# Kernel optimization log

Measured on AMD Instinct MI355X. Metric: run time of the kernel, lower is better.

The kernel has to match this reference:

```python
import jax, jax.numpy as jnp
import numpy as np

DK = 64

def setup_inputs() -> dict:
    key = jax.random.key(0)
    kx, kq, kk, kv = jax.random.split(key, 4)
    B, T, DM, DV = 256, 256, 384, 64
    x = jax.random.normal(kx, (B, T, DM), dtype=jnp.float32)
    s = 1.0 / np.sqrt(DM)
    W_q = jax.random.normal(kq, (DM, DK), dtype=jnp.float32) * s
    W_k = jax.random.normal(kk, (DM, DK), dtype=jnp.float32) * s
    W_v = jax.random.normal(kv, (DM, DV), dtype=jnp.float32) * s
    return {"x": x, "W_q": W_q, "W_k": W_k, "W_v": W_v}

def reference(x, W_q, W_k, W_v):
    # x: [B, T, dm]; projections to [B, T, dk]/[B, T, dv]
    q = jnp.einsum('btc,ck->btk', x, W_q)
    k = jnp.einsum('btc,ck->btk', x, W_k)
    v = jnp.einsum('btc,cv->btv', x, W_v)
    scale = k.shape[-1] ** (-0.5)
    wei = jnp.einsum('btk,bsk->bts', q, k) * scale  # [B, T, T]
    T = x.shape[1]
    causal = jnp.tril(jnp.ones((T, T), dtype=bool))
    wei = jnp.where(causal, wei, -jnp.inf)
    wei = jax.nn.softmax(wei, axis=-1)
    # dropout omitted (eval mode / deterministic reference)
    out = jnp.einsum('bts,bsv->btv', wei, v)
    return out
```

## Files before the change

### kernel.cpp

```cpp
#include <hip/hip_runtime.h>


typedef __attribute__((ext_vector_type(8))) short short8;
typedef __attribute__((ext_vector_type(4))) float floatx4;

__device__ inline unsigned short f2bf(float f) {
  union { float f; unsigned u; } v; v.f = f;
  unsigned r = v.u + 0x7FFFu + ((v.u >> 16) & 1u);
  return (unsigned short)(r >> 16);
}

__device__ inline void glds16(const void* g, void* l) {
  __builtin_amdgcn_global_load_lds(
      (const __attribute__((address_space(1))) void*)g,
      (__attribute__((address_space(3))) void*)l, 16, 0, 0);
}

__global__ void wt_kernel(const float* __restrict__ wq, const float* __restrict__ wk,
                          const float* __restrict__ wv, unsigned short* __restrict__ wt) {
  int idx = blockIdx.x * 256 + threadIdx.x;
  if (idx >= 3 * 64 * 384) return;
  int mat = idx / (64 * 384);
  int rem = idx % (64 * 384);
  int n = rem / 384, k = rem % 384;
  const float* w = (mat == 0) ? wq : ((mat == 1) ? wk : wv);
  wt[idx] = f2bf(w[k * 64 + n]);
}

__global__ __launch_bounds__(1024) void fused_kernel(
    const float* __restrict__ x, const unsigned short* __restrict__ wt,
    float* __restrict__ out) {
  __shared__ __align__(16) unsigned short wb[2][3 * 192 * 32];
  __shared__ __align__(16) unsigned short sK[256 * 72];
  __shared__ __align__(16) unsigned short sVT[64 * 264];

  int tid = threadIdx.x, lane = tid & 63, w = tid >> 6;
  int m = lane & 15, q = lane >> 4;
  int b = blockIdx.x;
  const float* xb = x + (size_t)b * 256 * 384;

  auto stage = [&](int mega, int buf) {
#pragma unroll
    for (int t = 0; t < 3; ++t) {
      int i = w + 16 * t;
      if (i < 36) {
        int kc = i / 12, sub = i % 12;
        int c = sub * 16 + (lane >> 2), g = lane & 3;
        glds16(wt + (size_t)c * 384 + (mega * 3 + kc) * 32 + g * 8,
               (void*)&wb[buf][kc * 6144 + sub * 512]);
      }
    }
  };

  floatx4 z = {0.f, 0.f, 0.f, 0.f};
  floatx4 acc[12];
#pragma unroll
  for (int nt = 0; nt < 12; ++nt) acc[nt] = z;

  stage(0, 0);
#pragma unroll
  for (int mega = 0; mega < 4; ++mega) {
    int buf = mega & 1;
    __syncthreads();
    if (mega < 3) stage(mega + 1, buf ^ 1);

#pragma unroll
    for (int kc = 0; kc < 3; ++kc) {
      int ks = mega * 3 + kc;
      const float* ap = xb + (size_t)(w * 16 + m) * 384 + ks * 32 + q * 8;
      float4 f0 = *(const float4*)ap;
      float4 f1 = *(const float4*)(ap + 4);
      short8 af;
      af[0] = (short)f2bf(f0.x); af[1] = (short)f2bf(f0.y);
      af[2] = (short)f2bf(f0.z); af[3] = (short)f2bf(f0.w);
      af[4] = (short)f2bf(f1.x); af[5] = (short)f2bf(f1.y);
      af[6] = (short)f2bf(f1.z); af[7] = (short)f2bf(f1.w);

      const unsigned short* wbk = &wb[buf][kc * 6144];
#pragma unroll
      for (int nt = 0; nt < 12; ++nt) {
        short8 bf = *(const short8*)&wbk[(nt * 16 + m) * 32 + q * 8];
        acc[nt] = __builtin_amdgcn_mfma_f32_16x16x32_bf16(af, bf, acc[nt], 0, 0, 0);
      }
    }
  }

  unsigned short* scr = &wb[0][0] + w * 1152;
#pragma unroll
  for (int nt = 0; nt < 8; ++nt) {
#pragma unroll
    for (int j = 0; j < 4; ++j) {
      unsigned short val = f2bf(acc[nt][j]);
      int lrow = q * 4 + j;
      if (nt < 4) scr[lrow * 72 + nt * 16 + m] = val;
      else        sK[(w * 16 + lrow) * 72 + (nt - 4) * 16 + m] = val;
    }
  }
#pragma unroll
  for (int nt = 8; nt < 12; ++nt) {
    ushort4 pv;
    pv.x = f2bf(acc[nt][0]); pv.y = f2bf(acc[nt][1]);
    pv.z = f2bf(acc[nt][2]); pv.w = f2bf(acc[nt][3]);
    *(ushort4*)&sVT[((nt - 8) * 16 + m) * 264 + w * 16 + q * 4] = pv;
  }

  short8 qf0 = *(const short8*)(scr + m * 72 + q * 8);
  short8 qf1 = *(const short8*)(scr + m * 72 + 32 + q * 8);

  __syncthreads();

  floatx4 sacc[16];
#pragma unroll
  for (int nt = 0; nt < 16; ++nt) {
    if (nt > w) continue;
    short8 kb0 = *(const short8*)(sK + (nt * 16 + m) * 72 + q * 8);
    short8 kb1 = *(const short8*)(sK + (nt * 16 + m) * 72 + 32 + q * 8);
    floatx4 t = __builtin_amdgcn_mfma_f32_16x16x32_bf16(qf0, kb0, z, 0, 0, 0);
    sacc[nt] = __builtin_amdgcn_mfma_f32_16x16x32_bf16(qf1, kb1, t, 0, 0, 0);
  }

  const float CSC = 0.18033688011112042f;
  float inv_[4];
  int rbase = w * 16 + q * 4;
#pragma unroll
  for (int j = 0; j < 4; ++j) {
    int rg = rbase + j;
    float sum = 0.f;
#pragma unroll
    for (int nt = 0; nt < 16; ++nt) {
      if (nt > w) continue;
      int col = nt * 16 + m;
      float p = (col <= rg) ? exp2f(sacc[nt][j] * CSC) : 0.f;
      sacc[nt][j] = p;
      sum += p;
    }
    sum += __shfl_xor(sum, 1);
    sum += __shfl_xor(sum, 2);
    sum += __shfl_xor(sum, 4);
    sum += __shfl_xor(sum, 8);
    inv_[j] = 1.f / sum;
  }

  floatx4 o[4];
#pragma unroll
  for (int vt = 0; vt < 4; ++vt) o[vt] = z;
#pragma unroll
  for (int c = 0; c < 4; ++c) {
    if (4 * c > w) continue;
#pragma unroll
    for (int t = 0; t < 4; ++t) {
      int nt = 4 * c + t;
#pragma unroll
      for (int j = 0; j < 4; ++j) {
        unsigned short pv = (nt <= w) ? f2bf(sacc[nt][j] * inv_[j]) : (unsigned short)0;
        scr[(q * 4 + j) * 72 + t * 16 + m] = pv;
      }
    }
    short8 pf0 = *(const short8*)(scr + m * 72 + q * 8);
    short8 pf1 = *(const short8*)(scr + m * 72 + 32 + q * 8);
#pragma unroll
    for (int vt = 0; vt < 4; ++vt) {
      short8 vb0 = *(const short8*)(sVT + (vt * 16 + m) * 264 + c * 64 + q * 8);
      short8 vb1 = *(const short8*)(sVT + (vt * 16 + m) * 264 + c * 64 + 32 + q * 8);
      o[vt] = __builtin_amdgcn_mfma_f32_16x16x32_bf16(pf0, vb0, o[vt], 0, 0, 0);
      o[vt] = __builtin_amdgcn_mfma_f32_16x16x32_bf16(pf1, vb1, o[vt], 0, 0, 0);
    }
  }

  float* op = out + ((size_t)b * 256 + w * 16) * 64;
#pragma unroll
  for (int vt = 0; vt < 4; ++vt)
#pragma unroll
    for (int j = 0; j < 4; ++j)
      op[(q * 4 + j) * 64 + vt * 16 + m] = o[vt][j];
}

extern "C" void kernel_launch(void* const* d_in, const int* in_sizes, int n_in,
                              void* d_out, int out_size, void* d_ws, size_t ws_size,
                              hipStream_t stream) {
  const float* x  = (const float*)d_in[0];
  const float* wq = (const float*)d_in[1];
  const float* wk = (const float*)d_in[2];
  const float* wv = (const float*)d_in[3];
  float* out = (float*)d_out;

  unsigned short* wt = (unsigned short*)d_ws;

  wt_kernel<<<288, 256, 0, stream>>>(wq, wk, wv, wt);
  fused_kernel<<<256, 1024, 0, stream>>>(x, wt, out);
}
```

Measured before the change: 171.4 us.

## Split fused attention into QKV projection and load-balanced attention kernels

```diff
diff --git a/kernel.cpp b/kernel.cpp
--- a/kernel.cpp
+++ b/kernel.cpp
@@ -27,28 +27,24 @@
   wt[idx] = f2bf(w[k * 64 + n]);
 }
 
-__global__ __launch_bounds__(1024) void fused_kernel(
+__global__ __launch_bounds__(256, 4) void qkv_kernel(
     const float* __restrict__ x, const unsigned short* __restrict__ wt,
-    float* __restrict__ out) {
-  __shared__ __align__(16) unsigned short wb[2][3 * 192 * 32];
-  __shared__ __align__(16) unsigned short sK[256 * 72];
-  __shared__ __align__(16) unsigned short sVT[64 * 264];
+    unsigned short* __restrict__ Qg, unsigned short* __restrict__ Kg,
+    unsigned short* __restrict__ VTg) {
+  __shared__ __align__(16) unsigned short wb[2][6144];
 
   int tid = threadIdx.x, lane = tid & 63, w = tid >> 6;
   int m = lane & 15, q = lane >> 4;
-  int b = blockIdx.x;
-  const float* xb = x + (size_t)b * 256 * 384;
-
-  auto stage = [&](int mega, int buf) {
+  size_t R0 = (size_t)blockIdx.x * 64;
+  const float* ap0 = x + (R0 + (size_t)(w * 16 + m)) * 384 + q * 8;
+
+  auto stage = [&](int ks, int buf) {
 #pragma unroll
     for (int t = 0; t < 3; ++t) {
-      int i = w + 16 * t;
-      if (i < 36) {
-        int kc = i / 12, sub = i % 12;
-        int c = sub * 16 + (lane >> 2), g = lane & 3;
-        glds16(wt + (size_t)c * 384 + (mega * 3 + kc) * 32 + g * 8,
-               (void*)&wb[buf][kc * 6144 + sub * 512]);
-      }
+      int sub = w * 3 + t;
+      int c = sub * 16 + (lane >> 2), g = lane & 3;
+      glds16(wt + (size_t)c * 384 + ks * 32 + g * 8,
+             (void*)&wb[buf][sub * 512]);
     }
   };
 
@@ -59,120 +55,130 @@
 
   stage(0, 0);
 #pragma unroll
-  for (int mega = 0; mega < 4; ++mega) {
-    int buf = mega & 1;
+  for (int ks = 0; ks < 12; ++ks) {
+    int buf = ks & 1;
     __syncthreads();
-    if (mega < 3) stage(mega + 1, buf ^ 1);
-
-#pragma unroll
-    for (int kc = 0; kc < 3; ++kc) {
-      int ks = mega * 3 + kc;
-      const float* ap = xb + (size_t)(w * 16 + m) * 384 + ks * 32 + q * 8;
-      float4 f0 = *(const float4*)ap;
-      float4 f1 = *(const float4*)(ap + 4);
-      short8 af;
-      af[0] = (short)f2bf(f0.x); af[1] = (short)f2bf(f0.y);
-      af[2] = (short)f2bf(f0.z); af[3] = (short)f2bf(f0.w);
-      af[4] = (short)f2bf(f1.x); af[5] = (short)f2bf(f1.y);
-      af[6] = (short)f2bf(f1.z); af[7] = (short)f2bf(f1.w);
-
-      const unsigned short* wbk = &wb[buf][kc * 6144];
-#pragma unroll
-      for (int nt = 0; nt < 12; ++nt) {
-        short8 bf = *(const short8*)&wbk[(nt * 16 + m) * 32 + q * 8];
-        acc[nt] = __builtin_amdgcn_mfma_f32_16x16x32_bf16(af, bf, acc[nt], 0, 0, 0);
-      }
-    }
-  }
+    if (ks < 11) stage(ks + 1, buf ^ 1);
+
+    float4 f0 = *(const float4*)(ap0 + ks * 32);
+    float4 f1 = *(const float4*)(ap0 + ks * 32 + 4);
+    short8 af;
+    af[0] = (short)f2bf(f0.x); af[1] = (short)f2bf(f0.y);
+    af[2] = (short)f2bf(f0.z); af[3] = (short)f2bf(f0.w);
+    af[4] = (short)f2bf(f1.x); af[5] = (short)f2bf(f1.y);
+    af[6] = (short)f2bf(f1.z); af[7] = (short)f2bf(f1.w);
+
+#pragma unroll
+    for (int nt = 0; nt < 12; ++nt) {
+      short8 bf = *(const short8*)&wb[buf][(nt * 16 + m) * 32 + q * 8];
+      acc[nt] = __builtin_amdgcn_mfma_f32_16x16x32_bf16(af, bf, acc[nt], 0, 0, 0);
+    }
+  }
+  __syncthreads();
 
   unsigned short* scr = &wb[0][0] + w * 1152;
 #pragma unroll
-  for (int nt = 0; nt < 8; ++nt) {
-#pragma unroll
-    for (int j = 0; j < 4; ++j) {
-      unsigned short val = f2bf(acc[nt][j]);
-      int lrow = q * 4 + j;
-      if (nt < 4) scr[lrow * 72 + nt * 16 + m] = val;
-      else        sK[(w * 16 + lrow) * 72 + (nt - 4) * 16 + m] = val;
-    }
-  }
+  for (int pass = 0; pass < 2; ++pass) {
+#pragma unroll
+    for (int nt = 0; nt < 4; ++nt) {
+#pragma unroll
+      for (int j = 0; j < 4; ++j)
+        scr[(q * 4 + j) * 72 + nt * 16 + m] = f2bf(acc[pass * 4 + nt][j]);
+    }
+    unsigned short* dst = (pass == 0 ? Qg : Kg) + (R0 + (size_t)(w * 16)) * 64;
+#pragma unroll
+    for (int pr = 0; pr < 2; ++pr) {
+      int sr = pr * 8 + (lane >> 3);
+      short8 row = *(const short8*)(scr + sr * 72 + (lane & 7) * 8);
+      *(short8*)(dst + sr * 64 + (lane & 7) * 8) = row;
+    }
+  }
+
+  int bb = (int)(R0 >> 8);
+  int tok0 = (int)(R0 & 255) + w * 16 + q * 4;
 #pragma unroll
   for (int nt = 8; nt < 12; ++nt) {
     ushort4 pv;
     pv.x = f2bf(acc[nt][0]); pv.y = f2bf(acc[nt][1]);
     pv.z = f2bf(acc[nt][2]); pv.w = f2bf(acc[nt][3]);
-    *(ushort4*)&sVT[((nt - 8) * 16 + m) * 264 + w * 16 + q * 4] = pv;
-  }
-
-  short8 qf0 = *(const short8*)(scr + m * 72 + q * 8);
-  short8 qf1 = *(const short8*)(scr + m * 72 + 32 + q * 8);
-
-  __syncthreads();
-
-  floatx4 sacc[16];
-#pragma unroll
-  for (int nt = 0; nt < 16; ++nt) {
-    if (nt > w) continue;
-    short8 kb0 = *(const short8*)(sK + (nt * 16 + m) * 72 + q * 8);
-    short8 kb1 = *(const short8*)(sK + (nt * 16 + m) * 72 + 32 + q * 8);
-    floatx4 t = __builtin_amdgcn_mfma_f32_16x16x32_bf16(qf0, kb0, z, 0, 0, 0);
-    sacc[nt] = __builtin_amdgcn_mfma_f32_16x16x32_bf16(qf1, kb1, t, 0, 0, 0);
-  }
+    *(ushort4*)(VTg + ((size_t)bb * 64 + (nt - 8) * 16 + m) * 256 + tok0) = pv;
+  }
+}
+
+__global__ __launch_bounds__(256, 4) void attn_kernel(
+    const unsigned short* __restrict__ Qg, const unsigned short* __restrict__ Kg,
+    const unsigned short* __restrict__ VTg, float* __restrict__ out) {
+  __shared__ __align__(16) unsigned short ps[4][640];
+
+  int tid = threadIdx.x, lane = tid & 63, w = tid >> 6;
+  int m = lane & 15, q = lane >> 4;
+  int b = blockIdx.x >> 2, qd = blockIdx.x & 3;
+  int r = (w >> 1) * 8 + ((w & 1) ? 7 - qd : qd);
+
+  const unsigned short* Qb = Qg + ((size_t)b * 256 + r * 16) * 64;
+  const unsigned short* Kb = Kg + (size_t)b * 256 * 64;
+  const unsigned short* Vb = VTg + (size_t)b * 64 * 256;
+  unsigned short* scr = ps[w];
+
+  short8 qf0 = *(const short8*)(Qb + m * 64 + q * 8);
+  short8 qf1 = *(const short8*)(Qb + m * 64 + 32 + q * 8);
+
+  floatx4 z = {0.f, 0.f, 0.f, 0.f};
+  floatx4 o[4];
+#pragma unroll
+  for (int vt = 0; vt < 4; ++vt) o[vt] = z;
+  float sum[4] = {0.f, 0.f, 0.f, 0.f};
 
   const float CSC = 0.18033688011112042f;
+  int rg = r * 16 + q * 4;
+  int np = (r >> 1) + 1;
+
+  for (int p = 0; p < np; ++p) {
+    const unsigned short* k0 = Kb + (size_t)(2 * p) * 16 * 64;
+    short8 ka0 = *(const short8*)(k0 + m * 64 + q * 8);
+    short8 ka1 = *(const short8*)(k0 + m * 64 + 32 + q * 8);
+    short8 kb0 = *(const short8*)(k0 + (16 + m) * 64 + q * 8);
+    short8 kb1 = *(const short8*)(k0 + (16 + m) * 64 + 32 + q * 8);
+    floatx4 s0 = __builtin_amdgcn_mfma_f32_16x16x32_bf16(qf0, ka0, z, 0, 0, 0);
+    s0 = __builtin_amdgcn_mfma_f32_16x16x32_bf16(qf1, ka1, s0, 0, 0, 0);
+    floatx4 s1 = __builtin_amdgcn_mfma_f32_16x16x32_bf16(qf0, kb0, z, 0, 0, 0);
+    s1 = __builtin_amdgcn_mfma_f32_16x16x32_bf16(qf1, kb1, s1, 0, 0, 0);
+
+    int c0 = 2 * p * 16 + m;
+#pragma unroll
+    for (int j = 0; j < 4; ++j) {
+      float p0 = (c0 <= rg + j) ? exp2f(s0[j] * CSC) : 0.f;
+      float p1 = (c0 + 16 <= rg + j) ? exp2f(s1[j] * CSC) : 0.f;
+      sum[j] += p0 + p1;
+      scr[(q * 4 + j) * 40 + m] = f2bf(p0);
+      scr[(q * 4 + j) * 40 + 16 + m] = f2bf(p1);
+    }
+    short8 pf = *(const short8*)(scr + m * 40 + q * 8);
+    const unsigned short* vp = Vb + p * 32 + q * 8;
+#pragma unroll
+    for (int vt = 0; vt < 4; ++vt) {
+      short8 vb = *(const short8*)(vp + (size_t)(vt * 16 + m) * 256);
+      o[vt] = __builtin_amdgcn_mfma_f32_16x16x32_bf16(pf, vb, o[vt], 0, 0, 0);
+    }
+  }
+
   float inv_[4];
-  int rbase = w * 16 + q * 4;
 #pragma unroll
   for (int j = 0; j < 4; ++j) {
-    int rg = rbase + j;
-    float sum = 0.f;
-#pragma unroll
-    for (int nt = 0; nt < 16; ++nt) {
-      if (nt > w) continue;
-      int col = nt * 16 + m;
-      float p = (col <= rg) ? exp2f(sacc[nt][j] * CSC) : 0.f;
-      sacc[nt][j] = p;
-      sum += p;
-    }
-    sum += __shfl_xor(sum, 1);
-    sum += __shfl_xor(sum, 2);
-    sum += __shfl_xor(sum, 4);
-    sum += __shfl_xor(sum, 8);
-    inv_[j] = 1.f / sum;
-  }
-
-  floatx4 o[4];
-#pragma unroll
-  for (int vt = 0; vt < 4; ++vt) o[vt] = z;
-#pragma unroll
-  for (int c = 0; c < 4; ++c) {
-    if (4 * c > w) continue;
-#pragma unroll
-    for (int t = 0; t < 4; ++t) {
-      int nt = 4 * c + t;
-#pragma unroll
-      for (int j = 0; j < 4; ++j) {
-        unsigned short pv = (nt <= w) ? f2bf(sacc[nt][j] * inv_[j]) : (unsigned short)0;
-        scr[(q * 4 + j) * 72 + t * 16 + m] = pv;
-      }
-    }
-    short8 pf0 = *(const short8*)(scr + m * 72 + q * 8);
-    short8 pf1 = *(const short8*)(scr + m * 72 + 32 + q * 8);
-#pragma unroll
-    for (int vt = 0; vt < 4; ++vt) {
-      short8 vb0 = *(const short8*)(sVT + (vt * 16 + m) * 264 + c * 64 + q * 8);
-      short8 vb1 = *(const short8*)(sVT + (vt * 16 + m) * 264 + c * 64 + 32 + q * 8);
-      o[vt] = __builtin_amdgcn_mfma_f32_16x16x32_bf16(pf0, vb0, o[vt], 0, 0, 0);
-      o[vt] = __builtin_amdgcn_mfma_f32_16x16x32_bf16(pf1, vb1, o[vt], 0, 0, 0);
-    }
-  }
-
-  float* op = out + ((size_t)b * 256 + w * 16) * 64;
+    float s = sum[j];
+    s += __shfl_xor(s, 1);
+    s += __shfl_xor(s, 2);
+    s += __shfl_xor(s, 4);
+    s += __shfl_xor(s, 8);
+    inv_[j] = 1.f / s;
+  }
+
+  float* op = out + ((size_t)b * 256 + r * 16) * 64;
 #pragma unroll
   for (int vt = 0; vt < 4; ++vt)
 #pragma unroll
     for (int j = 0; j < 4; ++j)
-      op[(q * 4 + j) * 64 + vt * 16 + m] = o[vt][j];
+      op[(q * 4 + j) * 64 + vt * 16 + m] = o[vt][j] * inv_[j];
 }
 
 extern "C" void kernel_launch(void* const* d_in, const int* in_sizes, int n_in,
@@ -184,8 +190,13 @@
   const float* wv = (const float*)d_in[3];
   float* out = (float*)d_out;
 
-  unsigned short* wt = (unsigned short*)d_ws;
+  unsigned char* ws = (unsigned char*)d_ws;
+  unsigned short* wt = (unsigned short*)ws;
+  unsigned short* Qg = (unsigned short*)(ws + (1u << 20));
+  unsigned short* Kg = (unsigned short*)(ws + (1u << 20) + (1u << 23));
+  unsigned short* VTg = (unsigned short*)(ws + (1u << 20) + (2u << 23));
 
   wt_kernel<<<288, 256, 0, stream>>>(wq, wk, wv, wt);
-  fused_kernel<<<256, 1024, 0, stream>>>(x, wt, out);
-}
+  qkv_kernel<<<1024, 256, 0, stream>>>(x, wt, Qg, Kg, VTg);
+  attn_kernel<<<1024, 256, 0, stream>>>(Qg, Kg, VTg, out);
+}
```

New measurement: 194.7 us. 1.14x slower.

## Split each batch across two 512-thread blocks with balanced causal row-tile pairing

Applied to the files above, without the earlier changes.

```diff
diff --git a/kernel.cpp b/kernel.cpp
--- a/kernel.cpp
+++ b/kernel.cpp
@@ -27,108 +27,134 @@
   wt[idx] = f2bf(w[k * 64 + n]);
 }
 
-__global__ __launch_bounds__(1024) void fused_kernel(
+__global__ __launch_bounds__(512, 4) void fused_kernel(
     const float* __restrict__ x, const unsigned short* __restrict__ wt,
     float* __restrict__ out) {
-  __shared__ __align__(16) unsigned short wb[2][3 * 192 * 32];
-  __shared__ __align__(16) unsigned short sK[256 * 72];
-  __shared__ __align__(16) unsigned short sVT[64 * 264];
+  __shared__ __align__(16) unsigned short U[37888];
 
   int tid = threadIdx.x, lane = tid & 63, w = tid >> 6;
   int m = lane & 15, q = lane >> 4;
-  int b = blockIdx.x;
+
+  int i = blockIdx.x;
+  int xcd = i & 7, jj = i >> 3;
+  int b = xcd * 32 + (jj >> 1);
+  int h = jj & 1;
   const float* xb = x + (size_t)b * 256 * 384;
 
-  auto stage = [&](int mega, int buf) {
-#pragma unroll
-    for (int t = 0; t < 3; ++t) {
-      int i = w + 16 * t;
-      if (i < 36) {
-        int kc = i / 12, sub = i % 12;
+  int ta = 2 * w + ((w ^ h) & 1);
+  int tb = 4 * w + 1 - ta;
+
+  auto stage = [&](int ks, int buf) {
+#pragma unroll
+    for (int t = 0; t < 2; ++t) {
+      int sub = w + 8 * t;
+      if (sub < 12) {
         int c = sub * 16 + (lane >> 2), g = lane & 3;
-        glds16(wt + (size_t)c * 384 + (mega * 3 + kc) * 32 + g * 8,
-               (void*)&wb[buf][kc * 6144 + sub * 512]);
+        glds16(wt + (size_t)c * 384 + ks * 32 + g * 8,
+               (void*)&U[buf * 6144 + sub * 512]);
       }
     }
   };
 
   floatx4 z = {0.f, 0.f, 0.f, 0.f};
-  floatx4 acc[12];
-#pragma unroll
-  for (int nt = 0; nt < 12; ++nt) acc[nt] = z;
+  floatx4 aA[12], aB[8];
+#pragma unroll
+  for (int nt = 0; nt < 12; ++nt) aA[nt] = z;
+#pragma unroll
+  for (int nt = 0; nt < 8; ++nt) aB[nt] = z;
+
+  const float* rowa = xb + (size_t)(ta * 16 + m) * 384 + q * 8;
+  const float* rowb = xb + (size_t)(tb * 16 + m) * 384 + q * 8;
 
   stage(0, 0);
 #pragma unroll
-  for (int mega = 0; mega < 4; ++mega) {
-    int buf = mega & 1;
+  for (int ks = 0; ks < 12; ++ks) {
+    int buf = ks & 1;
     __syncthreads();
-    if (mega < 3) stage(mega + 1, buf ^ 1);
-
-#pragma unroll
-    for (int kc = 0; kc < 3; ++kc) {
-      int ks = mega * 3 + kc;
-      const float* ap = xb + (size_t)(w * 16 + m) * 384 + ks * 32 + q * 8;
-      float4 f0 = *(const float4*)ap;
-      float4 f1 = *(const float4*)(ap + 4);
-      short8 af;
-      af[0] = (short)f2bf(f0.x); af[1] = (short)f2bf(f0.y);
-      af[2] = (short)f2bf(f0.z); af[3] = (short)f2bf(f0.w);
-      af[4] = (short)f2bf(f1.x); af[5] = (short)f2bf(f1.y);
-      af[6] = (short)f2bf(f1.z); af[7] = (short)f2bf(f1.w);
-
-      const unsigned short* wbk = &wb[buf][kc * 6144];
-#pragma unroll
-      for (int nt = 0; nt < 12; ++nt) {
-        short8 bf = *(const short8*)&wbk[(nt * 16 + m) * 32 + q * 8];
-        acc[nt] = __builtin_amdgcn_mfma_f32_16x16x32_bf16(af, bf, acc[nt], 0, 0, 0);
-      }
-    }
-  }
-
-  unsigned short* scr = &wb[0][0] + w * 1152;
-#pragma unroll
-  for (int nt = 0; nt < 8; ++nt) {
+    if (ks < 11) stage(ks + 1, buf ^ 1);
+
+    float4 a0 = *(const float4*)(rowa + ks * 32);
+    float4 a1 = *(const float4*)(rowa + ks * 32 + 4);
+    float4 b0 = *(const float4*)(rowb + ks * 32);
+    float4 b1 = *(const float4*)(rowb + ks * 32 + 4);
+    short8 afA, afB;
+    afA[0] = (short)f2bf(a0.x); afA[1] = (short)f2bf(a0.y);
+    afA[2] = (short)f2bf(a0.z); afA[3] = (short)f2bf(a0.w);
+    afA[4] = (short)f2bf(a1.x); afA[5] = (short)f2bf(a1.y);
+    afA[6] = (short)f2bf(a1.z); afA[7] = (short)f2bf(a1.w);
+    afB[0] = (short)f2bf(b0.x); afB[1] = (short)f2bf(b0.y);
+    afB[2] = (short)f2bf(b0.z); afB[3] = (short)f2bf(b0.w);
+    afB[4] = (short)f2bf(b1.x); afB[5] = (short)f2bf(b1.y);
+    afB[6] = (short)f2bf(b1.z); afB[7] = (short)f2bf(b1.w);
+
+#pragma unroll
+    for (int nt = 0; nt < 12; ++nt) {
+      short8 bf = *(const short8*)&U[buf * 6144 + (nt * 16 + m) * 32 + q * 8];
+      aA[nt] = __builtin_amdgcn_mfma_f32_16x16x32_bf16(afA, bf, aA[nt], 0, 0, 0);
+      if (nt >= 4)
+        aB[nt - 4] = __builtin_amdgcn_mfma_f32_16x16x32_bf16(afB, bf, aB[nt - 4], 0, 0, 0);
+    }
+  }
+
+  unsigned short* qs = U + 16384 + w * 1152;
+#pragma unroll
+  for (int nt = 0; nt < 4; ++nt)
+#pragma unroll
+    for (int j = 0; j < 4; ++j)
+      qs[(q * 4 + j) * 72 + nt * 16 + m] = f2bf(aA[nt][j]);
+  short8 qf0 = *(const short8*)(qs + m * 72 + q * 8);
+  short8 qf1 = *(const short8*)(qs + m * 72 + 32 + q * 8);
+
+  __syncthreads();
+
+  char* Uc = (char*)U;
+#pragma unroll
+  for (int n4 = 0; n4 < 4; ++n4) {
 #pragma unroll
     for (int j = 0; j < 4; ++j) {
-      unsigned short val = f2bf(acc[nt][j]);
-      int lrow = q * 4 + j;
-      if (nt < 4) scr[lrow * 72 + nt * 16 + m] = val;
-      else        sK[(w * 16 + lrow) * 72 + (nt - 4) * 16 + m] = val;
-    }
-  }
-#pragma unroll
-  for (int nt = 8; nt < 12; ++nt) {
-    ushort4 pv;
-    pv.x = f2bf(acc[nt][0]); pv.y = f2bf(acc[nt][1]);
-    pv.z = f2bf(acc[nt][2]); pv.w = f2bf(acc[nt][3]);
-    *(ushort4*)&sVT[((nt - 8) * 16 + m) * 264 + w * 16 + q * 4] = pv;
-  }
-
-  short8 qf0 = *(const short8*)(scr + m * 72 + q * 8);
-  short8 qf1 = *(const short8*)(scr + m * 72 + 32 + q * 8);
+      int ra = ta * 16 + q * 4 + j, ca = n4 * 16 + m;
+      int bya = (ra * 128 + ca * 2) ^ ((ra & 7) << 4);
+      *(unsigned short*)(Uc + bya) = f2bf(aA[4 + n4][j]);
+      int rb = tb * 16 + q * 4 + j;
+      int byb = (rb * 128 + ca * 2) ^ ((rb & 7) << 4);
+      *(unsigned short*)(Uc + byb) = f2bf(aB[n4][j]);
+    }
+    int vrow = n4 * 16 + m;
+    ushort4 pa, pb;
+    pa.x = f2bf(aA[8 + n4][0]); pa.y = f2bf(aA[8 + n4][1]);
+    pa.z = f2bf(aA[8 + n4][2]); pa.w = f2bf(aA[8 + n4][3]);
+    pb.x = f2bf(aB[4 + n4][0]); pb.y = f2bf(aB[4 + n4][1]);
+    pb.z = f2bf(aB[4 + n4][2]); pb.w = f2bf(aB[4 + n4][3]);
+    int bva = (vrow * 512 + (ta * 16 + q * 4) * 2) ^ ((vrow & 7) << 4);
+    int bvb = (vrow * 512 + (tb * 16 + q * 4) * 2) ^ ((vrow & 7) << 4);
+    *(ushort4*)(Uc + 32768 + bva) = pa;
+    *(ushort4*)(Uc + 32768 + bvb) = pb;
+  }
 
   __syncthreads();
 
+  int r = ta;
   floatx4 sacc[16];
 #pragma unroll
   for (int nt = 0; nt < 16; ++nt) {
-    if (nt > w) continue;
-    short8 kb0 = *(const short8*)(sK + (nt * 16 + m) * 72 + q * 8);
-    short8 kb1 = *(const short8*)(sK + (nt * 16 + m) * 72 + 32 + q * 8);
+    if (nt > r) continue;
+    int by0 = (((nt * 16 + m) * 128) + q * 16) ^ ((m & 7) << 4);
+    short8 kb0 = *(const short8*)(Uc + by0);
+    short8 kb1 = *(const short8*)(Uc + (by0 ^ 64));
     floatx4 t = __builtin_amdgcn_mfma_f32_16x16x32_bf16(qf0, kb0, z, 0, 0, 0);
     sacc[nt] = __builtin_amdgcn_mfma_f32_16x16x32_bf16(qf1, kb1, t, 0, 0, 0);
   }
 
   const float CSC = 0.18033688011112042f;
   float inv_[4];
-  int rbase = w * 16 + q * 4;
+  int rbase = r * 16 + q * 4;
 #pragma unroll
   for (int j = 0; j < 4; ++j) {
     int rg = rbase + j;
     float sum = 0.f;
 #pragma unroll
     for (int nt = 0; nt < 16; ++nt) {
-      if (nt > w) continue;
+      if (nt > r) continue;
       int col = nt * 16 + m;
       float p = (col <= rg) ? exp2f(sacc[nt][j] * CSC) : 0.f;
       sacc[nt][j] = p;
@@ -141,33 +167,32 @@
     inv_[j] = 1.f / sum;
   }
 
+  unsigned short* ps = U + 32768 + w * 640;
   floatx4 o[4];
 #pragma unroll
   for (int vt = 0; vt < 4; ++vt) o[vt] = z;
 #pragma unroll
-  for (int c = 0; c < 4; ++c) {
-    if (4 * c > w) continue;
-#pragma unroll
-    for (int t = 0; t < 4; ++t) {
-      int nt = 4 * c + t;
+  for (int c2 = 0; c2 < 8; ++c2) {
+    if (2 * c2 > r) continue;
+#pragma unroll
+    for (int t = 0; t < 2; ++t) {
+      int nt = 2 * c2 + t;
 #pragma unroll
       for (int j = 0; j < 4; ++j) {
-        unsigned short pv = (nt <= w) ? f2bf(sacc[nt][j] * inv_[j]) : (unsigned short)0;
-        scr[(q * 4 + j) * 72 + t * 16 + m] = pv;
+        unsigned short pv = (nt <= r) ? f2bf(sacc[nt][j] * inv_[j]) : (unsigned short)0;
+        ps[(q * 4 + j) * 40 + t * 16 + m] = pv;
       }
     }
-    short8 pf0 = *(const short8*)(scr + m * 72 + q * 8);
-    short8 pf1 = *(const short8*)(scr + m * 72 + 32 + q * 8);
+    short8 pf = *(const short8*)(ps + m * 40 + q * 8);
 #pragma unroll
     for (int vt = 0; vt < 4; ++vt) {
-      short8 vb0 = *(const short8*)(sVT + (vt * 16 + m) * 264 + c * 64 + q * 8);
-      short8 vb1 = *(const short8*)(sVT + (vt * 16 + m) * 264 + c * 64 + 32 + q * 8);
-      o[vt] = __builtin_amdgcn_mfma_f32_16x16x32_bf16(pf0, vb0, o[vt], 0, 0, 0);
-      o[vt] = __builtin_amdgcn_mfma_f32_16x16x32_bf16(pf1, vb1, o[vt], 0, 0, 0);
-    }
-  }
-
-  float* op = out + ((size_t)b * 256 + w * 16) * 64;
+      int bv = (((vt * 16 + m) * 512) + c2 * 64 + q * 16) ^ ((m & 7) << 4);
+      short8 vb = *(const short8*)(Uc + 32768 + bv);
+      o[vt] = __builtin_amdgcn_mfma_f32_16x16x32_bf16(pf, vb, o[vt], 0, 0, 0);
+    }
+  }
+
+  float* op = out + ((size_t)b * 256 + r * 16) * 64;
 #pragma unroll
   for (int vt = 0; vt < 4; ++vt)
 #pragma unroll
@@ -187,5 +212,5 @@
   unsigned short* wt = (unsigned short*)d_ws;
 
   wt_kernel<<<288, 256, 0, stream>>>(wq, wk, wv, wt);
-  fused_kernel<<<256, 1024, 0, stream>>>(x, wt, out);
-}
+  fused_kernel<<<512, 512, 0, stream>>>(x, wt, out);
+}
```

Result: slower. 184.7 us (+7.8%).

## Retile QKV projection to 32x96 per wave to reuse weight fragments

Applied to the files above, without the earlier changes.

```diff
diff --git a/kernel.cpp b/kernel.cpp
--- a/kernel.cpp
+++ b/kernel.cpp
@@ -36,6 +36,7 @@
 
   int tid = threadIdx.x, lane = tid & 63, w = tid >> 6;
   int m = lane & 15, q = lane >> 4;
+  int rg = w >> 1, cg = w & 1;
   int b = blockIdx.x;
   const float* xb = x + (size_t)b * 256 * 384;
 
@@ -53,9 +54,11 @@
   };
 
   floatx4 z = {0.f, 0.f, 0.f, 0.f};
-  floatx4 acc[12];
-#pragma unroll
-  for (int nt = 0; nt < 12; ++nt) acc[nt] = z;
+  floatx4 acc[2][6];
+#pragma unroll
+  for (int j = 0; j < 2; ++j)
+#pragma unroll
+    for (int t = 0; t < 6; ++t) acc[j][t] = z;
 
   stage(0, 0);
 #pragma unroll
@@ -67,47 +70,72 @@
 #pragma unroll
     for (int kc = 0; kc < 3; ++kc) {
       int ks = mega * 3 + kc;
-      const float* ap = xb + (size_t)(w * 16 + m) * 384 + ks * 32 + q * 8;
-      float4 f0 = *(const float4*)ap;
-      float4 f1 = *(const float4*)(ap + 4);
-      short8 af;
-      af[0] = (short)f2bf(f0.x); af[1] = (short)f2bf(f0.y);
-      af[2] = (short)f2bf(f0.z); af[3] = (short)f2bf(f0.w);
-      af[4] = (short)f2bf(f1.x); af[5] = (short)f2bf(f1.y);
-      af[6] = (short)f2bf(f1.z); af[7] = (short)f2bf(f1.w);
-
       const unsigned short* wbk = &wb[buf][kc * 6144];
-#pragma unroll
-      for (int nt = 0; nt < 12; ++nt) {
-        short8 bf = *(const short8*)&wbk[(nt * 16 + m) * 32 + q * 8];
-        acc[nt] = __builtin_amdgcn_mfma_f32_16x16x32_bf16(af, bf, acc[nt], 0, 0, 0);
-      }
-    }
-  }
-
-  unsigned short* scr = &wb[0][0] + w * 1152;
-#pragma unroll
-  for (int nt = 0; nt < 8; ++nt) {
-#pragma unroll
-    for (int j = 0; j < 4; ++j) {
-      unsigned short val = f2bf(acc[nt][j]);
-      int lrow = q * 4 + j;
-      if (nt < 4) scr[lrow * 72 + nt * 16 + m] = val;
-      else        sK[(w * 16 + lrow) * 72 + (nt - 4) * 16 + m] = val;
-    }
-  }
-#pragma unroll
-  for (int nt = 8; nt < 12; ++nt) {
-    ushort4 pv;
-    pv.x = f2bf(acc[nt][0]); pv.y = f2bf(acc[nt][1]);
-    pv.z = f2bf(acc[nt][2]); pv.w = f2bf(acc[nt][3]);
-    *(ushort4*)&sVT[((nt - 8) * 16 + m) * 264 + w * 16 + q * 4] = pv;
-  }
-
-  short8 qf0 = *(const short8*)(scr + m * 72 + q * 8);
-  short8 qf1 = *(const short8*)(scr + m * 72 + 32 + q * 8);
+
+      short8 af0, af1;
+      {
+        const float* ap = xb + (size_t)(rg * 32 + m) * 384 + ks * 32 + q * 8;
+        float4 f0 = *(const float4*)ap;
+        float4 f1 = *(const float4*)(ap + 4);
+        af0[0] = (short)f2bf(f0.x); af0[1] = (short)f2bf(f0.y);
+        af0[2] = (short)f2bf(f0.z); af0[3] = (short)f2bf(f0.w);
+        af0[4] = (short)f2bf(f1.x); af0[5] = (short)f2bf(f1.y);
+        af0[6] = (short)f2bf(f1.z); af0[7] = (short)f2bf(f1.w);
+      }
+      {
+        const float* ap = xb + (size_t)(rg * 32 + 16 + m) * 384 + ks * 32 + q * 8;
+        float4 f0 = *(const float4*)ap;
+        float4 f1 = *(const float4*)(ap + 4);
+        af1[0] = (short)f2bf(f0.x); af1[1] = (short)f2bf(f0.y);
+        af1[2] = (short)f2bf(f0.z); af1[3] = (short)f2bf(f0.w);
+        af1[4] = (short)f2bf(f1.x); af1[5] = (short)f2bf(f1.y);
+        af1[6] = (short)f2bf(f1.z); af1[7] = (short)f2bf(f1.w);
+      }
+
+#pragma unroll
+      for (int t = 0; t < 6; ++t) {
+        short8 bf = *(const short8*)&wbk[((cg * 6 + t) * 16 + m) * 32 + q * 8];
+        acc[0][t] = __builtin_amdgcn_mfma_f32_16x16x32_bf16(af0, bf, acc[0][t], 0, 0, 0);
+        acc[1][t] = __builtin_amdgcn_mfma_f32_16x16x32_bf16(af1, bf, acc[1][t], 0, 0, 0);
+      }
+    }
+  }
+
+  unsigned short* sQ = &wb[0][0];
+#pragma unroll
+  for (int j = 0; j < 2; ++j) {
+    int rb2 = rg * 32 + j * 16 + q * 4;
+    if (cg == 0) {
+#pragma unroll
+      for (int t = 0; t < 4; ++t)
+#pragma unroll
+        for (int jj = 0; jj < 4; ++jj)
+          sQ[(rb2 + jj) * 72 + t * 16 + m] = f2bf(acc[j][t][jj]);
+#pragma unroll
+      for (int t = 4; t < 6; ++t)
+#pragma unroll
+        for (int jj = 0; jj < 4; ++jj)
+          sK[(rb2 + jj) * 72 + (t - 4) * 16 + m] = f2bf(acc[j][t][jj]);
+    } else {
+#pragma unroll
+      for (int t = 0; t < 2; ++t)
+#pragma unroll
+        for (int jj = 0; jj < 4; ++jj)
+          sK[(rb2 + jj) * 72 + (t + 2) * 16 + m] = f2bf(acc[j][t][jj]);
+#pragma unroll
+      for (int t = 2; t < 6; ++t) {
+        ushort4 pv;
+        pv.x = f2bf(acc[j][t][0]); pv.y = f2bf(acc[j][t][1]);
+        pv.z = f2bf(acc[j][t][2]); pv.w = f2bf(acc[j][t][3]);
+        *(ushort4*)&sVT[((t - 2) * 16 + m) * 264 + rb2] = pv;
+      }
+    }
+  }
 
   __syncthreads();
+
+  short8 qf0 = *(const short8*)(sQ + (w * 16 + m) * 72 + q * 8);
+  short8 qf1 = *(const short8*)(sQ + (w * 16 + m) * 72 + 32 + q * 8);
 
   floatx4 sacc[16];
 #pragma unroll
@@ -124,13 +152,13 @@
   int rbase = w * 16 + q * 4;
 #pragma unroll
   for (int j = 0; j < 4; ++j) {
-    int rg = rbase + j;
+    int rg2 = rbase + j;
     float sum = 0.f;
 #pragma unroll
     for (int nt = 0; nt < 16; ++nt) {
       if (nt > w) continue;
       int col = nt * 16 + m;
-      float p = (col <= rg) ? exp2f(sacc[nt][j] * CSC) : 0.f;
+      float p = (col <= rg2) ? exp2f(sacc[nt][j] * CSC) : 0.f;
       sacc[nt][j] = p;
       sum += p;
     }
@@ -141,6 +169,7 @@
     inv_[j] = 1.f / sum;
   }
 
+  unsigned short* scr = &wb[1][0] + w * 1152;
   floatx4 o[4];
 #pragma unroll
   for (int vt = 0; vt < 4; ++vt) o[vt] = z;
```

After: 173.8 us. Within noise of the previous version (+1.4%).
